# Optimization experiments

Measured on AMD Instinct MI355X. Metric: run time of the kernel, lower is better.

Reference implementation:

```python
import jax, jax.numpy as jnp
import numpy as np

N, E, IN_DIM, H, C = 100000, 1600000, 128, 4, 64
NEG_SLOPE = 0.2
BN_EPS = 1e-5


def setup_inputs() -> dict:
    key = jax.random.key(0)
    ks = jax.random.split(key, 9)
    s = 1.0 / np.sqrt(IN_DIM)
    return {
        "feature": jax.random.normal(ks[0], (N, IN_DIM), dtype=jnp.float32),
        "edge_index": jax.random.randint(ks[1], (2, E), 0, N, dtype=jnp.int64),
        "W_l": jax.random.uniform(ks[2], (IN_DIM, H * C), jnp.float32, -s, s),
        "b_l": jnp.zeros((H * C,), jnp.float32),
        "W_r": jax.random.uniform(ks[3], (IN_DIM, H * C), jnp.float32, -s, s),
        "b_r": jnp.zeros((H * C,), jnp.float32),
        "att": jax.random.normal(ks[4], (H, C), dtype=jnp.float32) * 0.1,
        "bias": jnp.zeros((H * C,), jnp.float32),
        "gamma": jnp.ones((H * C,), jnp.float32),
        "beta": jnp.zeros((H * C,), jnp.float32),
    }


def reference(feature, edge_index, W_l, b_l, W_r, b_r, att, bias, gamma, beta):
    n = feature.shape[0]
    # add self loops (add_self_loops=True)
    loops = jnp.arange(n, dtype=edge_index.dtype)
    src = jnp.concatenate([edge_index[0], loops])
    dst = jnp.concatenate([edge_index[1], loops])
    # GATv2: separate source/target linear projections -> [N, H, C]
    x_l = (feature @ W_l + b_l).reshape(n, H, C)
    x_r = (feature @ W_r + b_r).reshape(n, H, C)
    # per-edge attention score: a^T LeakyReLU(x_l[src] + x_r[dst])  [Etot, H]
    e = jax.nn.leaky_relu(x_l[src] + x_r[dst], NEG_SLOPE)
    alpha = jnp.einsum('ehc,hc->eh', e, att)
    # segment softmax over incoming edges per target node
    amax = jax.ops.segment_max(alpha, dst, num_segments=n)  # [N, H]
    alpha = jnp.exp(alpha - amax[dst])
    denom = jax.ops.segment_sum(alpha, dst, num_segments=n)  # [N, H]
    alpha = alpha / (denom[dst] + 1e-16)
    # weighted scatter-aggregate of source messages
    out = jax.ops.segment_sum(x_l[src] * alpha[:, :, None], dst, num_segments=n)
    out = out.reshape(n, H * C) + bias  # concat=True
    # BatchNorm1d (training: batch statistics over nodes)
    mean = out.mean(axis=0)
    var = out.var(axis=0)
    out = (out - mean) / jnp.sqrt(var + BN_EPS) * gamma + beta
    return jax.nn.relu(out)
```

## Files before the change

kernel.cpp:

```cpp
#include <hip/hip_runtime.h>
#include <cstdint>

#define IN_DIM 128
#define HC 256
#define NEG_SLOPE 0.2f
#define BN_EPS 1e-5f
#define LOG2E 1.44269504088896340736f

#define B_HIST 1536
#define B_FILL 1024
#define NBUF 64
#define B_AGG 2048

typedef short bf16x8 __attribute__((ext_vector_type(8)));
typedef float f32x4 __attribute__((ext_vector_type(4)));

#define EXP2F(x) __builtin_amdgcn_exp2f(x)

__device__ __forceinline__ unsigned short f2bf(float f) {
    union { float f; unsigned int u; } v; v.f = f;
    unsigned int r = (v.u + 0x7FFFu + ((v.u >> 16) & 1u)) >> 16;
    return (unsigned short)r;
}
__device__ __forceinline__ float bf2f(unsigned short h) {
    union { unsigned int u; float f; } v; v.u = ((unsigned int)h) << 16;
    return v.f;
}

template<int CTRL>
__device__ __forceinline__ float dppadd(float x) {
    int y = __builtin_amdgcn_update_dpp(0, __builtin_bit_cast(int, x), CTRL, 0xF, 0xF, true);
    return x + __builtin_bit_cast(float, y);
}
__device__ __forceinline__ float red16(float p) {
    p = dppadd<0xB1>(p);
    p = dppadd<0x4E>(p);
    p = dppadd<0x124>(p);
    p = dppadd<0x128>(p);
    return p;
}

__device__ __forceinline__ void unpk(ushort4 u, float* f) {
    f[0] = bf2f(u.x); f[1] = bf2f(u.y); f[2] = bf2f(u.z); f[3] = bf2f(u.w);
}
__device__ __forceinline__ float esc(const float* f, float x0, float x1, float x2, float x3,
                                     float4 a) {
    float z0 = f[0] + x0, z1 = f[1] + x1, z2 = f[2] + x2, z3 = f[3] + x3;
    float p = a.x * fmaxf(z0, NEG_SLOPE * z0);
    p = fmaf(a.y, fmaxf(z1, NEG_SLOPE * z1), p);
    p = fmaf(a.z, fmaxf(z2, NEG_SLOPE * z2), p);
    p = fmaf(a.w, fmaxf(z3, NEG_SLOPE * z3), p);
    return p;
}

__global__ __launch_bounds__(256) void prep(
    const float* __restrict__ Wl, const float* __restrict__ Wr,
    unsigned short* __restrict__ Wfrag,
    int* __restrict__ cnt, float* __restrict__ partials, int n)
{
    int b = blockIdx.x;
    if (b < 32) {
        int ob = b * 4 + (threadIdx.x >> 6);
        int j = ob >> 2;
        int kk = ob & 3;
        int l = threadIdx.x & 63;
        int col = j * 16 + (l & 15);
        const float* W = (col < 256) ? Wl : Wr;
        int c = col & 255;
        unsigned short tmp[8];
#pragma unroll
        for (int m = 0; m < 8; ++m) {
            int k = kk * 32 + ((l >> 4) << 3) + m;
            tmp[m] = f2bf(W[(size_t)k * 256 + c]);
        }
        ulonglong2* dst = (ulonglong2*)(Wfrag + ((size_t)(j * 4 + kk) * 64 + l) * 8);
        *dst = *(ulonglong2*)tmp;
    } else {
        int idx = (b - 32) * 256 + threadIdx.x;
        int stride = 96 * 256;
        for (int i = idx; i < n; i += stride) cnt[i] = 0;
        for (int i = idx; i < NBUF * 1024; i += stride) partials[i] = 0.f;
    }
}

__global__ __launch_bounds__(256) void phase_hg(
    const float* __restrict__ F, const unsigned short* __restrict__ Wfrag,
    const float* __restrict__ bl, const float* __restrict__ br,
    unsigned short* __restrict__ xl, unsigned short* __restrict__ xr,
    const int* __restrict__ ei, int* __restrict__ cnt, int* __restrict__ rank,
    int E, int n, int ntiles)
{
    int b = blockIdx.x;
    if (b < B_HIST) {
        for (int e = b * 256 + threadIdx.x; e < E; e += B_HIST * 256) {
            int dst = ei[(size_t)E + e];
            rank[e] = atomicAdd(&cnt[dst], 1);
        }
        return;
    }
    int i = (b - B_HIST) * 4 + (threadIdx.x >> 6);
    if (i >= ntiles) return;
    int l = threadIdx.x & 63;

    int row = i * 16 + (l & 15);
    bf16x8 afr[4];
#pragma unroll
    for (int kk = 0; kk < 4; ++kk) {
        int k0 = kk * 32 + ((l >> 4) << 3);
        float4 f0 = make_float4(0.f, 0.f, 0.f, 0.f), f1 = f0;
        if (row < n) {
            const float* p = F + (size_t)row * IN_DIM + k0;
            f0 = *(const float4*)p;
            f1 = *(const float4*)(p + 4);
        }
        unsigned short tmp[8];
        tmp[0] = f2bf(f0.x); tmp[1] = f2bf(f0.y); tmp[2] = f2bf(f0.z); tmp[3] = f2bf(f0.w);
        tmp[4] = f2bf(f1.x); tmp[5] = f2bf(f1.y); tmp[6] = f2bf(f1.z); tmp[7] = f2bf(f1.w);
        afr[kk] = *(bf16x8*)tmp;
    }

    const bf16x8* wv = (const bf16x8*)Wfrag + l;
    int cl = l & 15;
    int rbase = i * 16 + ((l >> 4) << 2);

#pragma unroll 4
    for (int j = 0; j < 32; ++j) {
        const bf16x8* bp = wv + (size_t)j * 4 * 64;
        f32x4 acc = {0.f, 0.f, 0.f, 0.f};
        acc = __builtin_amdgcn_mfma_f32_16x16x32_bf16(afr[0], bp[0 * 64], acc, 0, 0, 0);
        acc = __builtin_amdgcn_mfma_f32_16x16x32_bf16(afr[1], bp[1 * 64], acc, 0, 0, 0);
        acc = __builtin_amdgcn_mfma_f32_16x16x32_bf16(afr[2], bp[2 * 64], acc, 0, 0, 0);
        acc = __builtin_amdgcn_mfma_f32_16x16x32_bf16(afr[3], bp[3 * 64], acc, 0, 0, 0);

        int col = j * 16 + cl;
        unsigned short* X = (col < 256) ? xl : xr;
        int c = col & 255;
        float bv = (col < 256) ? bl[c] : br[c];
#pragma unroll
        for (int q = 0; q < 4; ++q) {
            int r = rbase + q;
            if (r < n) X[(size_t)r * HC + c] = f2bf(acc[q] + bv);
        }
    }
}

#define SCAN_BLOCKS 256

__global__ __launch_bounds__(256) void scan_phaseA(const int* __restrict__ cnt,
                                                   int* __restrict__ blocksums,
                                                   int n, int ept)
{
    __shared__ int red[256];
    int t = threadIdx.x;
    int g = blockIdx.x * 256 + t;
    int beg = g * ept, end = min(beg + ept, n);
    int s = 0;
    for (int i = beg; i < end; ++i) s += cnt[i];
    red[t] = s;
    __syncthreads();
    for (int d = 128; d > 0; d >>= 1) {
        if (t < d) red[t] += red[t + d];
        __syncthreads();
    }
    if (t == 0) blocksums[blockIdx.x] = red[0];
}

__global__ __launch_bounds__(256) void scan_phaseC(const int* __restrict__ cnt,
                                                   const int* __restrict__ blocksums,
                                                   int* __restrict__ off,
                                                   int n, int ept)
{
    __shared__ int bs[256];
    __shared__ int sums[256];
    int t = threadIdx.x;
    bs[t] = blocksums[t];
    int g = blockIdx.x * 256 + t;
    int beg = g * ept, end = min(beg + ept, n);
    int s = 0;
    for (int i = beg; i < end; ++i) s += cnt[i];
    sums[t] = s;
    __syncthreads();
    for (int d = 1; d < 256; d <<= 1) {
        int v1 = (t >= d) ? sums[t - d] : 0;
        int v2 = (t >= d) ? bs[t - d] : 0;
        __syncthreads();
        sums[t] += v1;
        bs[t] += v2;
        __syncthreads();
    }
    int blockoff = (blockIdx.x == 0) ? 0 : bs[blockIdx.x - 1];
    int run = blockoff + ((t == 0) ? 0 : sums[t - 1]);
    for (int i = beg; i < end; ++i) {
        int c = cnt[i];
        off[i] = run;
        run += c;
    }
    if (blockIdx.x == 0 && t == 0) off[n] = bs[255];
}

__global__ void fill_kernel(const int* __restrict__ ei, const int* __restrict__ rank,
                            const int* __restrict__ off, int* __restrict__ csr_boff,
                            int E)
{
    for (int e = blockIdx.x * blockDim.x + threadIdx.x; e < E;
         e += gridDim.x * blockDim.x) {
        int src = ei[e];
        int dst = ei[(size_t)E + e];
        int pos = off[dst] + rank[e];
        csr_boff[pos] = src << 9;
    }
}

__global__ __launch_bounds__(256) void gat_agg(
    const unsigned short* __restrict__ xl, const unsigned short* __restrict__ xr,
    const int* __restrict__ csr_boff, const int* __restrict__ off,
    const float* __restrict__ att, const float* __restrict__ bias,
    unsigned short* __restrict__ outb, float* __restrict__ partials, int n)
{
    int gwave = blockIdx.x * 4 + (threadIdx.x >> 6);
    int nwaves = B_AGG * 4;
    int lane = threadIdx.x & 63;

    const char* xlc = (const char*)xl;
    int lo8 = lane << 3;
    float4 att4 = *(const float4*)(att + 4 * lane);
    att4.x *= LOG2E; att4.y *= LOG2E; att4.z *= LOG2E; att4.w *= LOG2E;
    float4 b4 = *(const float4*)(bias + 4 * lane);

    float bnS0 = 0.f, bnS1 = 0.f, bnS2 = 0.f, bnS3 = 0.f;
    float bnQ0 = 0.f, bnQ1 = 0.f, bnQ2 = 0.f, bnQ3 = 0.f;

    for (int d = gwave; d < n; d += nwaves) {
        ushort4 xru = ((const ushort4*)xr)[(size_t)d * 64 + lane];
        float xr0 = bf2f(xru.x), xr1 = bf2f(xru.y), xr2 = bf2f(xru.z), xr3 = bf2f(xru.w);

        int beg = __builtin_amdgcn_readfirstlane(off[d]);
        int end = __builtin_amdgcn_readfirstlane(off[d + 1]);

        float ax, ay, az, aw, lsum;
        {
            ushort4 t0 = *(const ushort4*)(xlc + ((size_t)d << 9) + lo8);
            float f0[4];
            unpk(t0, f0);
            float p0 = esc(f0, xr0, xr1, xr2, xr3, att4);
            p0 = red16(p0);
            float e0 = EXP2F(p0);
            ax = e0 * f0[0]; ay = e0 * f0[1]; az = e0 * f0[2]; aw = e0 * f0[3];
            lsum = e0;
        }

        int nmain = (end - beg) & ~3;
        int imend = beg + nmain;
        int i = beg;

        ushort4 u0, u1, u2, u3;
        if (i < imend) {
            int b0 = __builtin_amdgcn_readfirstlane(csr_boff[i]);
            int b1 = __builtin_amdgcn_readfirstlane(csr_boff[i + 1]);
            int b2 = __builtin_amdgcn_readfirstlane(csr_boff[i + 2]);
            int b3 = __builtin_amdgcn_readfirstlane(csr_boff[i + 3]);
            u0 = *(const ushort4*)(xlc + b0 + lo8);
            u1 = *(const ushort4*)(xlc + b1 + lo8);
            u2 = *(const ushort4*)(xlc + b2 + lo8);
            u3 = *(const ushort4*)(xlc + b3 + lo8);
        }
        while (i < imend) {
            ushort4 c0 = u0, c1 = u1, c2 = u2, c3 = u3;
            int inext = i + 4;
            if (inext < imend) {
                int b0 = __builtin_amdgcn_readfirstlane(csr_boff[inext]);
                int b1 = __builtin_amdgcn_readfirstlane(csr_boff[inext + 1]);
                int b2 = __builtin_amdgcn_readfirstlane(csr_boff[inext + 2]);
                int b3 = __builtin_amdgcn_readfirstlane(csr_boff[inext + 3]);
                u0 = *(const ushort4*)(xlc + b0 + lo8);
                u1 = *(const ushort4*)(xlc + b1 + lo8);
                u2 = *(const ushort4*)(xlc + b2 + lo8);
                u3 = *(const ushort4*)(xlc + b3 + lo8);
            }
            float f0[4], f1[4], f2[4], f3[4];
            unpk(c0, f0); unpk(c1, f1); unpk(c2, f2); unpk(c3, f3);

            float p0 = esc(f0, xr0, xr1, xr2, xr3, att4);
            float p1 = esc(f1, xr0, xr1, xr2, xr3, att4);
            float p2 = esc(f2, xr0, xr1, xr2, xr3, att4);
            float p3 = esc(f3, xr0, xr1, xr2, xr3, att4);

            p0 = dppadd<0xB1>(p0);  p1 = dppadd<0xB1>(p1);  p2 = dppadd<0xB1>(p2);  p3 = dppadd<0xB1>(p3);
            p0 = dppadd<0x4E>(p0);  p1 = dppadd<0x4E>(p1);  p2 = dppadd<0x4E>(p2);  p3 = dppadd<0x4E>(p3);
            p0 = dppadd<0x124>(p0); p1 = dppadd<0x124>(p1); p2 = dppadd<0x124>(p2); p3 = dppadd<0x124>(p3);
            p0 = dppadd<0x128>(p0); p1 = dppadd<0x128>(p1); p2 = dppadd<0x128>(p2); p3 = dppadd<0x128>(p3);

            float e0 = EXP2F(p0), e1 = EXP2F(p1);
            float e2 = EXP2F(p2), e3 = EXP2F(p3);
            ax = fmaf(e0, f0[0], fmaf(e1, f1[0], fmaf(e2, f2[0], fmaf(e3, f3[0], ax))));
            ay = fmaf(e0, f0[1], fmaf(e1, f1[1], fmaf(e2, f2[1], fmaf(e3, f3[1], ay))));
            az = fmaf(e0, f0[2], fmaf(e1, f1[2], fmaf(e2, f2[2], fmaf(e3, f3[2], az))));
            aw = fmaf(e0, f0[3], fmaf(e1, f1[3], fmaf(e2, f2[3], fmaf(e3, f3[3], aw))));
            lsum += (e0 + e1) + (e2 + e3);
            i = inext;
        }
        for (; i < end; ++i) {
            int b0 = __builtin_amdgcn_readfirstlane(csr_boff[i]);
            ushort4 t0 = *(const ushort4*)(xlc + b0 + lo8);
            float f0[4];
            unpk(t0, f0);
            float p0 = esc(f0, xr0, xr1, xr2, xr3, att4);
            p0 = red16(p0);
            float e0 = EXP2F(p0);
            ax = fmaf(e0, f0[0], ax); ay = fmaf(e0, f0[1], ay);
            az = fmaf(e0, f0[2], az); aw = fmaf(e0, f0[3], aw);
            lsum += e0;
        }

        float inv = 1.f / (lsum + 1e-16f);
        ushort4 o;
        o.x = f2bf(fmaf(ax, inv, b4.x));
        o.y = f2bf(fmaf(ay, inv, b4.y));
        o.z = f2bf(fmaf(az, inv, b4.z));
        o.w = f2bf(fmaf(aw, inv, b4.w));
        ((ushort4*)outb)[(size_t)d * 64 + lane] = o;
        float vx = bf2f(o.x), vy = bf2f(o.y), vz = bf2f(o.z), vw = bf2f(o.w);
        bnS0 += vx; bnS1 += vy; bnS2 += vz; bnS3 += vw;
        bnQ0 = fmaf(vx, vx, bnQ0); bnQ1 = fmaf(vy, vy, bnQ1);
        bnQ2 = fmaf(vz, vz, bnQ2); bnQ3 = fmaf(vw, vw, bnQ3);
    }

    float* pb = partials + (size_t)(gwave & (NBUF - 1)) * 1024;
    int c0 = lane << 2;
    atomicAdd(&pb[c0 + 0], bnS0);
    atomicAdd(&pb[c0 + 1], bnS1);
    atomicAdd(&pb[c0 + 2], bnS2);
    atomicAdd(&pb[c0 + 3], bnS3);
    atomicAdd(&pb[512 + c0 + 0], bnQ0);
    atomicAdd(&pb[512 + c0 + 1], bnQ1);
    atomicAdd(&pb[512 + c0 + 2], bnQ2);
    atomicAdd(&pb[512 + c0 + 3], bnQ3);
}

__global__ __launch_bounds__(256) void bn_final(const float* __restrict__ partials,
                                                float* __restrict__ stats, int n)
{
    int c = threadIdx.x;
    float s = 0.f, s2 = 0.f;
    for (int b = 0; b < NBUF; ++b) {
        s  += partials[(size_t)b * 1024 + c];
        s2 += partials[(size_t)b * 1024 + 512 + c];
    }
    float mean = s / (float)n;
    float var = s2 / (float)n - mean * mean;
    stats[c] = mean;
    stats[256 + c] = rsqrtf(var + BN_EPS);
}

__global__ void bn_apply(const unsigned short* __restrict__ outb,
                         const float* __restrict__ stats,
                         const float* __restrict__ gamma, const float* __restrict__ beta,
                         float* __restrict__ out, long long total4)
{
    long long stride = (long long)gridDim.x * blockDim.x;
    for (long long i = blockIdx.x * (long long)blockDim.x + threadIdx.x; i < total4;
         i += stride) {
        int cb = ((int)(i & 63)) * 4;
        ushort4 u = ((const ushort4*)outb)[i];
        float4 o;
        o.x = fmaxf(0.f, (bf2f(u.x) - stats[cb + 0]) * stats[256 + cb + 0] * gamma[cb + 0] + beta[cb + 0]);
        o.y = fmaxf(0.f, (bf2f(u.y) - stats[cb + 1]) * stats[256 + cb + 1] * gamma[cb + 1] + beta[cb + 1]);
        o.z = fmaxf(0.f, (bf2f(u.z) - stats[cb + 2]) * stats[256 + cb + 2] * gamma[cb + 2] + beta[cb + 2]);
        o.w = fmaxf(0.f, (bf2f(u.w) - stats[cb + 3]) * stats[256 + cb + 3] * gamma[cb + 3] + beta[cb + 3]);
        ((float4*)out)[i] = o;
    }
}

extern "C" void kernel_launch(void* const* d_in, const int* in_sizes, int n_in,
                              void* d_out, int out_size, void* d_ws, size_t ws_size,
                              hipStream_t stream)
{
    const float* feature = (const float*)d_in[0];
    const int* ei        = (const int*)d_in[1];
    const float* Wl   = (const float*)d_in[2];
    const float* bl   = (const float*)d_in[3];
    const float* Wr   = (const float*)d_in[4];
    const float* br   = (const float*)d_in[5];
    const float* att  = (const float*)d_in[6];
    const float* bias = (const float*)d_in[7];
    const float* gamma = (const float*)d_in[8];
    const float* beta  = (const float*)d_in[9];

    const int n = in_sizes[0] / IN_DIM;
    const int E = in_sizes[1] / 2;
    const int ntiles = (n + 15) / 16;

    char* ws = (char*)d_ws;
    size_t o = 0;
    auto carve = [&](size_t bytes) -> void* {
        void* p = ws + o; o = (o + bytes + 15) & ~(size_t)15; return p;
    };
    unsigned short* xl    = (unsigned short*)carve((size_t)n * HC * sizeof(short));
    unsigned short* xr    = (unsigned short*)carve((size_t)n * HC * sizeof(short));
    unsigned short* outb  = (unsigned short*)carve((size_t)n * HC * sizeof(short));
    unsigned short* Wfrag = (unsigned short*)carve((size_t)32 * 4 * 64 * 8 * sizeof(short));
    int*   csr_boff = (int*)carve((size_t)E * sizeof(int));
    int*   rank    = (int*)carve((size_t)E * sizeof(int));
    int*   cnt     = (int*)carve((size_t)n * sizeof(int));
    int*   off     = (int*)carve((size_t)(n + 1) * sizeof(int));
    int*   blocksums = (int*)carve(SCAN_BLOCKS * sizeof(int));
    float* partials = (float*)carve((size_t)NBUF * 1024 * sizeof(float));
    float* stats   = (float*)carve(512 * sizeof(float));
    float* outf = (float*)d_out;

    if (o > ws_size) return;

    prep<<<128, 256, 0, stream>>>(Wl, Wr, Wfrag, cnt, partials, n);

    phase_hg<<<B_HIST + (ntiles + 3) / 4, 256, 0, stream>>>(
        feature, Wfrag, bl, br, xl, xr, ei, cnt, rank, E, n, ntiles);

    int ept = (n + SCAN_BLOCKS * 256 - 1) / (SCAN_BLOCKS * 256);
    scan_phaseA<<<SCAN_BLOCKS, 256, 0, stream>>>(cnt, blocksums, n, ept);
    scan_phaseC<<<SCAN_BLOCKS, 256, 0, stream>>>(cnt, blocksums, off, n, ept);

    fill_kernel<<<B_FILL, 256, 0, stream>>>(ei, rank, off, csr_boff, E);

    gat_agg<<<B_AGG, 256, 0, stream>>>(xl, xr, csr_boff, off, att, bias,
                                       outb, partials, n);

    bn_final<<<1, 256, 0, stream>>>(partials, stats, n);
    long long total4 = (long long)n * (HC / 4);
    bn_apply<<<4096, 256, 0, stream>>>(outb, stats, gamma, beta, outf, total4);
}
```

Baseline: 387.5 us.

## Launch one wave per node in aggregation and move BN stats to separate pass

The aggregation kernel now launches one wavefront per destination node instead of a fixed grid of persistent waves looping over nodes. The fused BatchNorm sum and sum-of-squares accumulation and its atomics are removed from it. A new bn_partial kernel rereads the bf16 output in 1024 row chunks to form per-block column partials, and bn_final becomes a 256-block tree reduction. This is meant to improve load balance and shorten the aggregation kernel, at the cost of an extra pass over the 51 MB output and one more launch.

```diff
diff --git a/kernel.cpp b/kernel.cpp
--- a/kernel.cpp
+++ b/kernel.cpp
@@ -9,8 +9,7 @@
 
 #define B_HIST 1536
 #define B_FILL 1024
-#define NBUF 64
-#define B_AGG 2048
+#define NB_BN 1024
 
 typedef short bf16x8 __attribute__((ext_vector_type(8)));
 typedef float f32x4 __attribute__((ext_vector_type(4)));
@@ -55,8 +54,7 @@
 
 __global__ __launch_bounds__(256) void prep(
     const float* __restrict__ Wl, const float* __restrict__ Wr,
-    unsigned short* __restrict__ Wfrag,
-    int* __restrict__ cnt, float* __restrict__ partials, int n)
+    unsigned short* __restrict__ Wfrag, int* __restrict__ cnt, int n)
 {
     int b = blockIdx.x;
     if (b < 32) {
@@ -79,7 +77,6 @@
         int idx = (b - 32) * 256 + threadIdx.x;
         int stride = 96 * 256;
         for (int i = idx; i < n; i += stride) cnt[i] = 0;
-        for (int i = idx; i < NBUF * 1024; i += stride) partials[i] = 0.f;
     }
 }
 
@@ -215,141 +212,147 @@
     const unsigned short* __restrict__ xl, const unsigned short* __restrict__ xr,
     const int* __restrict__ csr_boff, const int* __restrict__ off,
     const float* __restrict__ att, const float* __restrict__ bias,
-    unsigned short* __restrict__ outb, float* __restrict__ partials, int n)
-{
-    int gwave = blockIdx.x * 4 + (threadIdx.x >> 6);
-    int nwaves = B_AGG * 4;
+    unsigned short* __restrict__ outb, int n)
+{
+    int d = (blockIdx.x * blockDim.x + threadIdx.x) >> 6;
     int lane = threadIdx.x & 63;
+    if (d >= n) return;
 
     const char* xlc = (const char*)xl;
     int lo8 = lane << 3;
+    ushort4 xru = ((const ushort4*)xr)[(size_t)d * 64 + lane];
+    float xr0 = bf2f(xru.x), xr1 = bf2f(xru.y), xr2 = bf2f(xru.z), xr3 = bf2f(xru.w);
     float4 att4 = *(const float4*)(att + 4 * lane);
     att4.x *= LOG2E; att4.y *= LOG2E; att4.z *= LOG2E; att4.w *= LOG2E;
-    float4 b4 = *(const float4*)(bias + 4 * lane);
-
-    float bnS0 = 0.f, bnS1 = 0.f, bnS2 = 0.f, bnS3 = 0.f;
-    float bnQ0 = 0.f, bnQ1 = 0.f, bnQ2 = 0.f, bnQ3 = 0.f;
-
-    for (int d = gwave; d < n; d += nwaves) {
-        ushort4 xru = ((const ushort4*)xr)[(size_t)d * 64 + lane];
-        float xr0 = bf2f(xru.x), xr1 = bf2f(xru.y), xr2 = bf2f(xru.z), xr3 = bf2f(xru.w);
-
-        int beg = __builtin_amdgcn_readfirstlane(off[d]);
-        int end = __builtin_amdgcn_readfirstlane(off[d + 1]);
-
-        float ax, ay, az, aw, lsum;
-        {
-            ushort4 t0 = *(const ushort4*)(xlc + ((size_t)d << 9) + lo8);
-            float f0[4];
-            unpk(t0, f0);
-            float p0 = esc(f0, xr0, xr1, xr2, xr3, att4);
-            p0 = red16(p0);
-            float e0 = EXP2F(p0);
-            ax = e0 * f0[0]; ay = e0 * f0[1]; az = e0 * f0[2]; aw = e0 * f0[3];
-            lsum = e0;
-        }
-
-        int nmain = (end - beg) & ~3;
-        int imend = beg + nmain;
-        int i = beg;
-
-        ushort4 u0, u1, u2, u3;
-        if (i < imend) {
-            int b0 = __builtin_amdgcn_readfirstlane(csr_boff[i]);
-            int b1 = __builtin_amdgcn_readfirstlane(csr_boff[i + 1]);
-            int b2 = __builtin_amdgcn_readfirstlane(csr_boff[i + 2]);
-            int b3 = __builtin_amdgcn_readfirstlane(csr_boff[i + 3]);
+
+    int beg = __builtin_amdgcn_readfirstlane(off[d]);
+    int end = __builtin_amdgcn_readfirstlane(off[d + 1]);
+
+    float ax, ay, az, aw, lsum;
+    {
+        ushort4 t0 = *(const ushort4*)(xlc + ((size_t)d << 9) + lo8);
+        float f0[4];
+        unpk(t0, f0);
+        float p0 = esc(f0, xr0, xr1, xr2, xr3, att4);
+        p0 = red16(p0);
+        float e0 = EXP2F(p0);
+        ax = e0 * f0[0]; ay = e0 * f0[1]; az = e0 * f0[2]; aw = e0 * f0[3];
+        lsum = e0;
+    }
+
+    int nmain = (end - beg) & ~3;
+    int imend = beg + nmain;
+    int i = beg;
+
+    ushort4 u0, u1, u2, u3;
+    if (i < imend) {
+        int b0 = __builtin_amdgcn_readfirstlane(csr_boff[i]);
+        int b1 = __builtin_amdgcn_readfirstlane(csr_boff[i + 1]);
+        int b2 = __builtin_amdgcn_readfirstlane(csr_boff[i + 2]);
+        int b3 = __builtin_amdgcn_readfirstlane(csr_boff[i + 3]);
+        u0 = *(const ushort4*)(xlc + b0 + lo8);
+        u1 = *(const ushort4*)(xlc + b1 + lo8);
+        u2 = *(const ushort4*)(xlc + b2 + lo8);
+        u3 = *(const ushort4*)(xlc + b3 + lo8);
+    }
+    while (i < imend) {
+        ushort4 c0 = u0, c1 = u1, c2 = u2, c3 = u3;
+        int inext = i + 4;
+        if (inext < imend) {
+            int b0 = __builtin_amdgcn_readfirstlane(csr_boff[inext]);
+            int b1 = __builtin_amdgcn_readfirstlane(csr_boff[inext + 1]);
+            int b2 = __builtin_amdgcn_readfirstlane(csr_boff[inext + 2]);
+            int b3 = __builtin_amdgcn_readfirstlane(csr_boff[inext + 3]);
             u0 = *(const ushort4*)(xlc + b0 + lo8);
             u1 = *(const ushort4*)(xlc + b1 + lo8);
             u2 = *(const ushort4*)(xlc + b2 + lo8);
             u3 = *(const ushort4*)(xlc + b3 + lo8);
         }
-        while (i < imend) {
-            ushort4 c0 = u0, c1 = u1, c2 = u2, c3 = u3;
-            int inext = i + 4;
-            if (inext < imend) {
-                int b0 = __builtin_amdgcn_readfirstlane(csr_boff[inext]);
-                int b1 = __builtin_amdgcn_readfirstlane(csr_boff[inext + 1]);
-                int b2 = __builtin_amdgcn_readfirstlane(csr_boff[inext + 2]);
-                int b3 = __builtin_amdgcn_readfirstlane(csr_boff[inext + 3]);
-                u0 = *(const ushort4*)(xlc + b0 + lo8);
-                u1 = *(const ushort4*)(xlc + b1 + lo8);
-                u2 = *(const ushort4*)(xlc + b2 + lo8);
-                u3 = *(const ushort4*)(xlc + b3 + lo8);
-            }
-            float f0[4], f1[4], f2[4], f3[4];
-            unpk(c0, f0); unpk(c1, f1); unpk(c2, f2); unpk(c3, f3);
-
-            float p0 = esc(f0, xr0, xr1, xr2, xr3, att4);
-            float p1 = esc(f1, xr0, xr1, xr2, xr3, att4);
-            float p2 = esc(f2, xr0, xr1, xr2, xr3, att4);
-            float p3 = esc(f3, xr0, xr1, xr2, xr3, att4);
-
-            p0 = dppadd<0xB1>(p0);  p1 = dppadd<0xB1>(p1);  p2 = dppadd<0xB1>(p2);  p3 = dppadd<0xB1>(p3);
-            p0 = dppadd<0x4E>(p0);  p1 = dppadd<0x4E>(p1);  p2 = dppadd<0x4E>(p2);  p3 = dppadd<0x4E>(p3);
-            p0 = dppadd<0x124>(p0); p1 = dppadd<0x124>(p1); p2 = dppadd<0x124>(p2); p3 = dppadd<0x124>(p3);
-            p0 = dppadd<0x128>(p0); p1 = dppadd<0x128>(p1); p2 = dppadd<0x128>(p2); p3 = dppadd<0x128>(p3);
-
-            float e0 = EXP2F(p0), e1 = EXP2F(p1);
-            float e2 = EXP2F(p2), e3 = EXP2F(p3);
-            ax = fmaf(e0, f0[0], fmaf(e1, f1[0], fmaf(e2, f2[0], fmaf(e3, f3[0], ax))));
-            ay = fmaf(e0, f0[1], fmaf(e1, f1[1], fmaf(e2, f2[1], fmaf(e3, f3[1], ay))));
-            az = fmaf(e0, f0[2], fmaf(e1, f1[2], fmaf(e2, f2[2], fmaf(e3, f3[2], az))));
-            aw = fmaf(e0, f0[3], fmaf(e1, f1[3], fmaf(e2, f2[3], fmaf(e3, f3[3], aw))));
-            lsum += (e0 + e1) + (e2 + e3);
-            i = inext;
-        }
-        for (; i < end; ++i) {
-            int b0 = __builtin_amdgcn_readfirstlane(csr_boff[i]);
-            ushort4 t0 = *(const ushort4*)(xlc + b0 + lo8);
-            float f0[4];
-            unpk(t0, f0);
-            float p0 = esc(f0, xr0, xr1, xr2, xr3, att4);
-            p0 = red16(p0);
-            float e0 = EXP2F(p0);
-            ax = fmaf(e0, f0[0], ax); ay = fmaf(e0, f0[1], ay);
-            az = fmaf(e0, f0[2], az); aw = fmaf(e0, f0[3], aw);
-            lsum += e0;
-        }
-
-        float inv = 1.f / (lsum + 1e-16f);
-        ushort4 o;
-        o.x = f2bf(fmaf(ax, inv, b4.x));
-        o.y = f2bf(fmaf(ay, inv, b4.y));
-        o.z = f2bf(fmaf(az, inv, b4.z));
-        o.w = f2bf(fmaf(aw, inv, b4.w));
-        ((ushort4*)outb)[(size_t)d * 64 + lane] = o;
-        float vx = bf2f(o.x), vy = bf2f(o.y), vz = bf2f(o.z), vw = bf2f(o.w);
-        bnS0 += vx; bnS1 += vy; bnS2 += vz; bnS3 += vw;
-        bnQ0 = fmaf(vx, vx, bnQ0); bnQ1 = fmaf(vy, vy, bnQ1);
-        bnQ2 = fmaf(vz, vz, bnQ2); bnQ3 = fmaf(vw, vw, bnQ3);
-    }
-
-    float* pb = partials + (size_t)(gwave & (NBUF - 1)) * 1024;
-    int c0 = lane << 2;
-    atomicAdd(&pb[c0 + 0], bnS0);
-    atomicAdd(&pb[c0 + 1], bnS1);
-    atomicAdd(&pb[c0 + 2], bnS2);
-    atomicAdd(&pb[c0 + 3], bnS3);
-    atomicAdd(&pb[512 + c0 + 0], bnQ0);
-    atomicAdd(&pb[512 + c0 + 1], bnQ1);
-    atomicAdd(&pb[512 + c0 + 2], bnQ2);
-    atomicAdd(&pb[512 + c0 + 3], bnQ3);
+        float f0[4], f1[4], f2[4], f3[4];
+        unpk(c0, f0); unpk(c1, f1); unpk(c2, f2); unpk(c3, f3);
+
+        float p0 = esc(f0, xr0, xr1, xr2, xr3, att4);
+        float p1 = esc(f1, xr0, xr1, xr2, xr3, att4);
+        float p2 = esc(f2, xr0, xr1, xr2, xr3, att4);
+        float p3 = esc(f3, xr0, xr1, xr2, xr3, att4);
+
+        p0 = dppadd<0xB1>(p0);  p1 = dppadd<0xB1>(p1);  p2 = dppadd<0xB1>(p2);  p3 = dppadd<0xB1>(p3);
+        p0 = dppadd<0x4E>(p0);  p1 = dppadd<0x4E>(p1);  p2 = dppadd<0x4E>(p2);  p3 = dppadd<0x4E>(p3);
+        p0 = dppadd<0x124>(p0); p1 = dppadd<0x124>(p1); p2 = dppadd<0x124>(p2); p3 = dppadd<0x124>(p3);
+        p0 = dppadd<0x128>(p0); p1 = dppadd<0x128>(p1); p2 = dppadd<0x128>(p2); p3 = dppadd<0x128>(p3);
+
+        float e0 = EXP2F(p0), e1 = EXP2F(p1);
+        float e2 = EXP2F(p2), e3 = EXP2F(p3);
+        ax = fmaf(e0, f0[0], fmaf(e1, f1[0], fmaf(e2, f2[0], fmaf(e3, f3[0], ax))));
+        ay = fmaf(e0, f0[1], fmaf(e1, f1[1], fmaf(e2, f2[1], fmaf(e3, f3[1], ay))));
+        az = fmaf(e0, f0[2], fmaf(e1, f1[2], fmaf(e2, f2[2], fmaf(e3, f3[2], az))));
+        aw = fmaf(e0, f0[3], fmaf(e1, f1[3], fmaf(e2, f2[3], fmaf(e3, f3[3], aw))));
+        lsum += (e0 + e1) + (e2 + e3);
+        i = inext;
+    }
+    for (; i < end; ++i) {
+        int b0 = __builtin_amdgcn_readfirstlane(csr_boff[i]);
+        ushort4 t0 = *(const ushort4*)(xlc + b0 + lo8);
+        float f0[4];
+        unpk(t0, f0);
+        float p0 = esc(f0, xr0, xr1, xr2, xr3, att4);
+        p0 = red16(p0);
+        float e0 = EXP2F(p0);
+        ax = fmaf(e0, f0[0], ax); ay = fmaf(e0, f0[1], ay);
+        az = fmaf(e0, f0[2], az); aw = fmaf(e0, f0[3], aw);
+        lsum += e0;
+    }
+
+    float inv = 1.f / (lsum + 1e-16f);
+    float4 b4 = *(const float4*)(bias + 4 * lane);
+    ushort4 o;
+    o.x = f2bf(fmaf(ax, inv, b4.x));
+    o.y = f2bf(fmaf(ay, inv, b4.y));
+    o.z = f2bf(fmaf(az, inv, b4.z));
+    o.w = f2bf(fmaf(aw, inv, b4.w));
+    ((ushort4*)outb)[(size_t)d * 64 + lane] = o;
+}
+
+__global__ __launch_bounds__(256) void bn_partial(const unsigned short* __restrict__ outb,
+                                                  float* __restrict__ partials, int n)
+{
+    int c = threadIdx.x;
+    int b = blockIdx.x;
+    int chunk = (n + NB_BN - 1) / NB_BN;
+    int beg = b * chunk;
+    int end = min(beg + chunk, n);
+    float s = 0.f, s2 = 0.f;
+    for (int r = beg; r < end; ++r) {
+        float v = bf2f(outb[(size_t)r * HC + c]);
+        s += v; s2 += v * v;
+    }
+    partials[(size_t)b * 512 + c] = s;
+    partials[(size_t)b * 512 + 256 + c] = s2;
 }
 
 __global__ __launch_bounds__(256) void bn_final(const float* __restrict__ partials,
                                                 float* __restrict__ stats, int n)
 {
-    int c = threadIdx.x;
+    int c = blockIdx.x;
+    int t = threadIdx.x;
     float s = 0.f, s2 = 0.f;
-    for (int b = 0; b < NBUF; ++b) {
-        s  += partials[(size_t)b * 1024 + c];
-        s2 += partials[(size_t)b * 1024 + 512 + c];
-    }
-    float mean = s / (float)n;
-    float var = s2 / (float)n - mean * mean;
-    stats[c] = mean;
-    stats[256 + c] = rsqrtf(var + BN_EPS);
+    for (int b = t; b < NB_BN; b += 256) {
+        s  += partials[(size_t)b * 512 + c];
+        s2 += partials[(size_t)b * 512 + 256 + c];
+    }
+    __shared__ float rs[256], rs2[256];
+    rs[t] = s; rs2[t] = s2;
+    __syncthreads();
+    for (int d = 128; d > 0; d >>= 1) {
+        if (t < d) { rs[t] += rs[t + d]; rs2[t] += rs2[t + d]; }
+        __syncthreads();
+    }
+    if (t == 0) {
+        float mean = rs[0] / (float)n;
+        float var = rs2[0] / (float)n - mean * mean;
+        stats[c] = mean;
+        stats[256 + c] = rsqrtf(var + BN_EPS);
+    }
 }
 
 __global__ void bn_apply(const unsigned short* __restrict__ outb,
@@ -404,13 +407,13 @@
     int*   cnt     = (int*)carve((size_t)n * sizeof(int));
     int*   off     = (int*)carve((size_t)(n + 1) * sizeof(int));
     int*   blocksums = (int*)carve(SCAN_BLOCKS * sizeof(int));
-    float* partials = (float*)carve((size_t)NBUF * 1024 * sizeof(float));
+    float* partials = (float*)carve((size_t)NB_BN * 512 * sizeof(float));
     float* stats   = (float*)carve(512 * sizeof(float));
     float* outf = (float*)d_out;
 
     if (o > ws_size) return;
 
-    prep<<<128, 256, 0, stream>>>(Wl, Wr, Wfrag, cnt, partials, n);
+    prep<<<128, 256, 0, stream>>>(Wl, Wr, Wfrag, cnt, n);
 
     phase_hg<<<B_HIST + (ntiles + 3) / 4, 256, 0, stream>>>(
         feature, Wfrag, bl, br, xl, xr, ei, cnt, rank, E, n, ntiles);
@@ -421,10 +424,11 @@
 
     fill_kernel<<<B_FILL, 256, 0, stream>>>(ei, rank, off, csr_boff, E);
 
-    gat_agg<<<B_AGG, 256, 0, stream>>>(xl, xr, csr_boff, off, att, bias,
-                                       outb, partials, n);
-
-    bn_final<<<1, 256, 0, stream>>>(partials, stats, n);
+    int agg_blocks = (n + 3) / 4;
+    gat_agg<<<agg_blocks, 256, 0, stream>>>(xl, xr, csr_boff, off, att, bias, outb, n);
+
+    bn_partial<<<NB_BN, 256, 0, stream>>>(outb, partials, n);
+    bn_final<<<256, 256, 0, stream>>>(partials, stats, n);
     long long total4 = (long long)n * (HC / 4);
     bn_apply<<<4096, 256, 0, stream>>>(outb, stats, gamma, beta, outf, total4);
 }
```

Measured after the change: 357.8 us. 7.7% less time.
